# Performance work log

Measured on AMD Instinct MI355X. Metric: run time of the kernel, lower is better.

## Reference

```python
import jax, jax.numpy as jnp
import numpy as np

B, S, D, H = 2, 2048, 2048, 16
DH = D // H  # 128


def setup_inputs() -> dict:
    key = jax.random.key(0)
    ks = jax.random.split(key, 7)
    x = jax.random.normal(ks[0], (B, S, D), dtype=jnp.float32)
    # causal mask [b, s, s], True = attend
    mask = jnp.broadcast_to(jnp.tril(jnp.ones((S, S), dtype=bool)), (B, S, S))
    scale = 1.0 / np.sqrt(D)
    Wq = jax.random.normal(ks[1], (D, H, DH), dtype=jnp.float32) * scale
    Wk = jax.random.normal(ks[2], (D, 1, DH), dtype=jnp.float32) * scale
    Wv = jax.random.normal(ks[3], (D, 1, DH), dtype=jnp.float32) * scale
    Wo = jax.random.normal(ks[4], (H, DH, D), dtype=jnp.float32) * scale
    bo = jnp.zeros((D,), dtype=jnp.float32)
    return {"x": x, "mask": mask, "Wq": Wq, "Wk": Wk, "Wv": Wv, "Wo": Wo, "bo": bo}


def reference(x, mask, Wq, Wk, Wv, Wo, bo):
    # projections: q [b,s,h,dh]; k,v [b,s,1,dh] (single shared KV head)
    q = jnp.einsum("bsd,dhe->bshe", x, Wq)
    k = jnp.einsum("bsd,dhe->bshe", x, Wk)[:, :, 0, :]  # [b,s,dh]
    v = jnp.einsum("bsd,dhe->bshe", x, Wv)[:, :, 0, :]  # [b,s,dh]
    # scores [b,h,s,s] with 1/sqrt(d_head) scaling
    scores = jnp.einsum("bqhe,bke->bhqk", q, k) / jnp.sqrt(
        jnp.asarray(q.shape[-1], dtype=q.dtype)
    )
    big_neg = jnp.finfo(scores.dtype).min
    scores = jnp.where(mask[:, None, :, :], scores, big_neg)
    probs = jax.nn.softmax(scores, axis=-1)
    attn = jnp.einsum("bhqk,bke->bhqe", probs, v)  # [b,h,s,dh]
    # output projection contracting (head, d_head) -> d_state, with bias
    out = jnp.einsum("bhqe,hed->bqd", attn, Wo) + bo
    return out
```

## Files before the change

### kernel.cpp

```cpp
#include <hip/hip_runtime.h>
#include <cmath>
#include <cstdint>

typedef __bf16 bf16;
typedef __bf16 bf16x8 __attribute__((ext_vector_type(8)));
typedef __bf16 bf16x4 __attribute__((ext_vector_type(4)));
typedef float f32x4 __attribute__((ext_vector_type(4)));

#define SDIM 2048
#define DDIM 2048
#define NQKV 2304
#define DH   128

__device__ __forceinline__ void glds16(const bf16* g, bf16* l) {
    __builtin_amdgcn_global_load_lds(
        (const __attribute__((address_space(1))) void*)g,
        (__attribute__((address_space(3))) void*)l, 16, 0, 0);
}

__global__ __launch_bounds__(256) void prep_kernel(const float* __restrict__ x,
                                                   const float* __restrict__ Wq,
                                                   const float* __restrict__ Wk,
                                                   const float* __restrict__ Wv,
                                                   const float* __restrict__ Wo,
                                                   bf16* __restrict__ xb,
                                                   bf16* __restrict__ Wqkv_t,
                                                   bf16* __restrict__ Wo_t) {
    __shared__ float tile[32][33];
    int bx = blockIdx.x;
    if (bx < 8192) {
        int i = bx * 256 + threadIdx.x;
        float4 v = reinterpret_cast<const float4*>(x)[i];
        bf16x4 o;
        o[0] = (bf16)v.x; o[1] = (bf16)v.y; o[2] = (bf16)v.z; o[3] = (bf16)v.w;
        reinterpret_cast<bf16x4*>(xb)[i] = o;
        return;
    }
    bx -= 8192;
    const float* src; bf16* dst; int srcN; int t;
    if (bx < 4096)      { src = Wq; dst = Wqkv_t;                      srcN = 2048; t = bx; }
    else if (bx < 4352) { src = Wk; dst = Wqkv_t + (size_t)2048*2048;  srcN = 128;  t = bx - 4096; }
    else if (bx < 4608) { src = Wv; dst = Wqkv_t + (size_t)2176*2048;  srcN = 128;  t = bx - 4352; }
    else                { src = Wo; dst = Wo_t;                        srcN = 2048; t = bx - 4608; }
    const int srcK = 2048;
    int ntx = srcN >> 5;
    int n0 = (t % ntx) * 32, k0 = (t / ntx) * 32;
    int tx = threadIdx.x & 31;
    int ty = threadIdx.x >> 5;
    for (int i = 0; i < 4; i++)
        tile[ty + i*8][tx] = src[(size_t)(k0 + ty + i*8) * srcN + n0 + tx];
    __syncthreads();
    for (int i = 0; i < 4; i++)
        dst[(size_t)(n0 + ty + i*8) * srcK + k0 + tx] = (bf16)tile[tx][ty + i*8];
}

__global__ __launch_bounds__(256) void vtrans_kernel(const bf16* __restrict__ QKV,
                                                     bf16* __restrict__ Vt) {
    __shared__ bf16 tile[32][33];
    int tx = threadIdx.x & 31;
    int ty = threadIdx.x >> 5;
    int d0 = blockIdx.x * 32;
    int s0 = blockIdx.y * 32;
    int b  = blockIdx.z;
    for (int i = 0; i < 4; i++)
        tile[ty + i*8][tx] = QKV[((size_t)b * SDIM + s0 + ty + i*8) * NQKV + 2176 + d0 + tx];
    __syncthreads();
    for (int i = 0; i < 4; i++)
        Vt[((size_t)b * DH + d0 + ty + i*8) * SDIM + s0 + tx] = tile[tx][ty + i*8];
}

template<int WRITE_F32>
__global__ __launch_bounds__(256) void gemm_bt_kernel(const bf16* __restrict__ A,
                                                      const bf16* __restrict__ Bt,
                                                      void* __restrict__ Cout,
                                                      const float* __restrict__ bias,
                                                      int K, int N) {
    __shared__ bf16 As[128 * 32];
    __shared__ bf16 Bs[128 * 32];
    const int tid  = threadIdx.x;
    const int wave = tid >> 6, lane = tid & 63;
    const int quad = lane >> 4, l15 = lane & 15;
    const int tm = blockIdx.x * 128, tn = blockIdx.y * 128;
    const int wm = (wave >> 1) * 64, wn = (wave & 1) * 64;

    const int lrow = lane >> 2, lcol = (lane & 3) * 8;
    const int wrow = wave * 32;
    const bf16* Ag0 = A  + (size_t)(tm + wrow + lrow)      * K + lcol;
    const bf16* Ag1 = A  + (size_t)(tm + wrow + 16 + lrow) * K + lcol;
    const bf16* Bg0 = Bt + (size_t)(tn + wrow + lrow)      * K + lcol;
    const bf16* Bg1 = Bt + (size_t)(tn + wrow + 16 + lrow) * K + lcol;
    bf16* Al0 = As + (wrow)      * 32;
    bf16* Al1 = As + (wrow + 16) * 32;
    bf16* Bl0 = Bs + (wrow)      * 32;
    bf16* Bl1 = Bs + (wrow + 16) * 32;

    f32x4 acc[4][4];
    for (int i = 0; i < 4; i++)
        for (int j = 0; j < 4; j++) acc[i][j] = (f32x4)0.0f;

    for (int k0 = 0; k0 < K; k0 += 32) {
        __syncthreads();
        glds16(Ag0 + k0, Al0);
        glds16(Ag1 + k0, Al1);
        glds16(Bg0 + k0, Bl0);
        glds16(Bg1 + k0, Bl1);
        __syncthreads();
        bf16x8 af[4], bfr[4];
        for (int i = 0; i < 4; i++)
            af[i]  = *reinterpret_cast<const bf16x8*>(As + (wm + i*16 + l15) * 32 + quad*8);
        for (int j = 0; j < 4; j++)
            bfr[j] = *reinterpret_cast<const bf16x8*>(Bs + (wn + j*16 + l15) * 32 + quad*8);
        for (int i = 0; i < 4; i++)
            for (int j = 0; j < 4; j++)
                acc[i][j] = __builtin_amdgcn_mfma_f32_16x16x32_bf16(af[i], bfr[j], acc[i][j], 0, 0, 0);
    }

    for (int i = 0; i < 4; i++)
        for (int j = 0; j < 4; j++)
            for (int r = 0; r < 4; r++) {
                int row = tm + wm + i*16 + quad*4 + r;
                int col = tn + wn + j*16 + l15;
                float v = acc[i][j][r];
                if (WRITE_F32)
                    reinterpret_cast<float*>(Cout)[(size_t)row * N + col] = v + bias[col];
                else
                    reinterpret_cast<bf16*>(Cout)[(size_t)row * N + col] = (bf16)v;
            }
}

#define FPLD 72

__global__ __launch_bounds__(512) void flash_kernel(const bf16* __restrict__ QKV,
                                                    const bf16* __restrict__ Vt,
                                                    bf16* __restrict__ attn) {
    __shared__ bf16 KVS[16384];
    __shared__ bf16 Ps[8 * 16 * FPLD];
    bf16* Ks  = KVS;
    bf16* Vts = KVS + 8192;

    const int tid  = threadIdx.x;
    const int wave = tid >> 6, lane = tid & 63;
    const int quad = lane >> 4, l15 = lane & 15;
    const int bx = blockIdx.x;
    const int qs = 255 - (bx >> 1);
    const int b  = bx & 1;
    const int q  = qs * 8 + wave;
    const size_t rowbase = (size_t)b * SDIM;
    const bf16* Vtb = Vt + (size_t)b * DH * SDIM;
    const float scale = 0.088388347648318447f;

    const int s0 = wave, s1 = wave + 8;
    const int krow0 = s0*4 + (lane >> 4), krow1 = s1*4 + (lane >> 4);
    const int kchunk = lane & 15;
    const bf16* kg0 = QKV + (rowbase + krow0) * NQKV + 2048 + ((kchunk ^ (krow0 & 15)) * 8);
    const bf16* kg1 = QKV + (rowbase + krow1) * NQKV + 2048 + ((kchunk ^ (krow1 & 15)) * 8);
    bf16* kl0 = Ks + s0 * 512;
    bf16* kl1 = Ks + s1 * 512;
    const int vrow0 = s0*8 + (lane >> 3), vrow1 = s1*8 + (lane >> 3);
    const int vchunk = lane & 7;
    const bf16* vg0 = Vtb + (size_t)vrow0 * SDIM + ((vchunk ^ (vrow0 & 7)) * 8);
    const bf16* vg1 = Vtb + (size_t)vrow1 * SDIM + ((vchunk ^ (vrow1 & 7)) * 8);
    bf16* vl0 = Vts + s0 * 512;
    bf16* vl1 = Vts + s1 * 512;

    bf16x8 qf[4];
    {
        const bf16* qp = QKV + (rowbase + q) * NQKV + l15 * DH + quad * 8;
        for (int kk = 0; kk < 4; kk++)
            qf[kk] = *reinterpret_cast<const bf16x8*>(qp + kk * 32);
    }
    float l_s[4] = {0.0f, 0.0f, 0.0f, 0.0f};
    f32x4 acc[8];
    for (int d = 0; d < 8; d++) acc[d] = (f32x4)0.0f;

    const int ntiles = (qs >> 3) + 1;
    bf16* Pw = Ps + wave * (16 * FPLD);

    const bf16* kp0 = kg0; const bf16* kp1 = kg1;
    const bf16* vp0 = vg0; const bf16* vp1 = vg1;

    for (int t = 0; t < ntiles; t++) {
        const int key0 = t * 64;
        __syncthreads();
        glds16(kp0, kl0); glds16(kp1, kl1);
        glds16(vp0, vl0); glds16(vp1, vl1);
        kp0 += 64 * NQKV; kp1 += 64 * NQKV; vp0 += 64; vp1 += 64;
        __syncthreads();

        f32x4 sc[4];
        for (int c = 0; c < 4; c++) sc[c] = (f32x4)0.0f;
        for (int c = 0; c < 4; c++)
            for (int kk = 0; kk < 4; kk++) {
                int j = (kk*4 + quad) ^ l15;
                bf16x8 kf = *reinterpret_cast<const bf16x8*>(
                    Ks + (c*16 + l15) * 128 + j * 8);
                sc[c] = __builtin_amdgcn_mfma_f32_16x16x32_bf16(qf[kk], kf, sc[c], 0, 0, 0);
            }

        const bool tail = (key0 + 63 > q);
        for (int c = 0; c < 4; c++)
            for (int r = 0; r < 4; r++) {
                float p;
                if (tail && (key0 + c*16 + l15 > q)) p = 0.0f;
                else p = __expf(sc[c][r] * scale);
                l_s[r] += p;
                Pw[(quad*4 + r) * FPLD + c*16 + l15] = (bf16)p;
            }

        for (int kk2 = 0; kk2 < 2; kk2++) {
            bf16x8 pf = *reinterpret_cast<const bf16x8*>(Pw + l15 * FPLD + kk2*32 + quad*8);
            for (int dd = 0; dd < 8; dd++) {
                int d = dd*16 + l15;
                int j = (kk2*4 + quad) ^ (l15 & 7);
                bf16x8 vf = *reinterpret_cast<const bf16x8*>(Vts + d * 64 + j * 8);
                acc[dd] = __builtin_amdgcn_mfma_f32_16x16x32_bf16(pf, vf, acc[dd], 0, 0, 0);
            }
        }
    }

    __syncthreads();

    for (int d = 1; d < 16; d <<= 1)
        for (int r = 0; r < 4; r++) l_s[r] += __shfl_xor(l_s[r], d);

    bf16* Ow = KVS + wave * 2048;
    for (int r = 0; r < 4; r++) {
        float inv = 1.0f / l_s[r];
        for (int d = 0; d < 8; d++)
            Ow[(quad*4 + r) * 128 + d*16 + l15] = (bf16)(acc[d][r] * inv);
    }
    const int orow = lane >> 2;
    const int ocol = (lane & 3) * 8;
    bf16* ob = attn + (rowbase + q) * (size_t)DDIM;
    for (int it = 0; it < 4; it++)
        *reinterpret_cast<uint4*>(ob + orow * DH + ocol + it*32) =
            *reinterpret_cast<const uint4*>(Ow + orow * 128 + ocol + it*32);
}

extern "C" void kernel_launch(void* const* d_in, const int* in_sizes, int n_in,
                              void* d_out, int out_size, void* d_ws, size_t ws_size,
                              hipStream_t stream) {
    const float* x  = (const float*)d_in[0];
    const float* Wq = (const float*)d_in[2];
    const float* Wk = (const float*)d_in[3];
    const float* Wv = (const float*)d_in[4];
    const float* Wo = (const float*)d_in[5];
    const float* bo = (const float*)d_in[6];
    float* out = (float*)d_out;

    char* ws = (char*)d_ws;
    bf16* xb     = (bf16*)(ws);
    bf16* Wqkv_t = (bf16*)(ws + 16777216);
    bf16* Wo_t   = (bf16*)(ws + 26214400);
    bf16* QKV    = (bf16*)(ws + 34603008);
    bf16* attn   = (bf16*)(ws + 53477376);
    bf16* Vtb    = (bf16*)(ws + 70254592);
    (void)ws_size; (void)in_sizes; (void)n_in; (void)out_size;

    prep_kernel<<<16896, 256, 0, stream>>>(x, Wq, Wk, Wv, Wo, xb, Wqkv_t, Wo_t);
    gemm_bt_kernel<0><<<dim3(32, 18), 256, 0, stream>>>(xb, Wqkv_t, (void*)QKV, nullptr, 2048, 2304);
    vtrans_kernel<<<dim3(4, 64, 2), 256, 0, stream>>>(QKV, Vtb);
    flash_kernel<<<512, 512, 0, stream>>>(QKV, Vtb, attn);
    gemm_bt_kernel<1><<<dim3(32, 16), 256, 0, stream>>>(attn, Wo_t, (void*)out, bo, 2048, 2048);
}
```

Baseline: 313.6 us.

## Double-buffer LDS tiles in GEMM and flash kernels; retile flash to 4 waves

Both the GEMM and the flash-attention kernels now use two LDS buffers. The next K/V (or A/B) tile is prefetched with global_load_lds while MFMAs work on the current one, which removes one barrier per iteration. The flash kernel also shrinks to 256 threads with 32-key tiles and 4 query rows per block, giving twice as many blocks. The costs are more LDS per block in the GEMM, smaller per-tile work in the flash kernel, and reliance on the barrier waiting for the async LDS loads to finish.

```diff
diff --git a/kernel.cpp b/kernel.cpp
--- a/kernel.cpp
+++ b/kernel.cpp
@@ -75,8 +75,8 @@
                                                       void* __restrict__ Cout,
                                                       const float* __restrict__ bias,
                                                       int K, int N) {
-    __shared__ bf16 As[128 * 32];
-    __shared__ bf16 Bs[128 * 32];
+    __shared__ bf16 As[2][128 * 32];
+    __shared__ bf16 Bs[2][128 * 32];
     const int tid  = threadIdx.x;
     const int wave = tid >> 6, lane = tid & 63;
     const int quad = lane >> 4, l15 = lane & 15;
@@ -89,27 +89,30 @@
     const bf16* Ag1 = A  + (size_t)(tm + wrow + 16 + lrow) * K + lcol;
     const bf16* Bg0 = Bt + (size_t)(tn + wrow + lrow)      * K + lcol;
     const bf16* Bg1 = Bt + (size_t)(tn + wrow + 16 + lrow) * K + lcol;
-    bf16* Al0 = As + (wrow)      * 32;
-    bf16* Al1 = As + (wrow + 16) * 32;
-    bf16* Bl0 = Bs + (wrow)      * 32;
-    bf16* Bl1 = Bs + (wrow + 16) * 32;
 
     f32x4 acc[4][4];
     for (int i = 0; i < 4; i++)
         for (int j = 0; j < 4; j++) acc[i][j] = (f32x4)0.0f;
 
+    glds16(Ag0, As[0] + wrow * 32);
+    glds16(Ag1, As[0] + (wrow + 16) * 32);
+    glds16(Bg0, Bs[0] + wrow * 32);
+    glds16(Bg1, Bs[0] + (wrow + 16) * 32);
+
     for (int k0 = 0; k0 < K; k0 += 32) {
+        const int buf = (k0 >> 5) & 1;
         __syncthreads();
-        glds16(Ag0 + k0, Al0);
-        glds16(Ag1 + k0, Al1);
-        glds16(Bg0 + k0, Bl0);
-        glds16(Bg1 + k0, Bl1);
-        __syncthreads();
+        if (k0 + 32 < K) {
+            glds16(Ag0 + k0 + 32, As[buf ^ 1] + wrow * 32);
+            glds16(Ag1 + k0 + 32, As[buf ^ 1] + (wrow + 16) * 32);
+            glds16(Bg0 + k0 + 32, Bs[buf ^ 1] + wrow * 32);
+            glds16(Bg1 + k0 + 32, Bs[buf ^ 1] + (wrow + 16) * 32);
+        }
         bf16x8 af[4], bfr[4];
         for (int i = 0; i < 4; i++)
-            af[i]  = *reinterpret_cast<const bf16x8*>(As + (wm + i*16 + l15) * 32 + quad*8);
+            af[i]  = *reinterpret_cast<const bf16x8*>(As[buf] + (wm + i*16 + l15) * 32 + quad*8);
         for (int j = 0; j < 4; j++)
-            bfr[j] = *reinterpret_cast<const bf16x8*>(Bs + (wn + j*16 + l15) * 32 + quad*8);
+            bfr[j] = *reinterpret_cast<const bf16x8*>(Bs[buf] + (wn + j*16 + l15) * 32 + quad*8);
         for (int i = 0; i < 4; i++)
             for (int j = 0; j < 4; j++)
                 acc[i][j] = __builtin_amdgcn_mfma_f32_16x16x32_bf16(af[i], bfr[j], acc[i][j], 0, 0, 0);
@@ -128,40 +131,36 @@
             }
 }
 
-#define FPLD 72
-
-__global__ __launch_bounds__(512) void flash_kernel(const bf16* __restrict__ QKV,
+#define FPLD 40
+
+__global__ __launch_bounds__(256) void flash_kernel(const bf16* __restrict__ QKV,
                                                     const bf16* __restrict__ Vt,
                                                     bf16* __restrict__ attn) {
-    __shared__ bf16 KVS[16384];
-    __shared__ bf16 Ps[8 * 16 * FPLD];
-    bf16* Ks  = KVS;
-    bf16* Vts = KVS + 8192;
+    __shared__ bf16 Ks[2][32 * 128];
+    __shared__ bf16 Vts[2][128 * 32];
+    __shared__ bf16 Ps[4 * 16 * FPLD];
 
     const int tid  = threadIdx.x;
     const int wave = tid >> 6, lane = tid & 63;
     const int quad = lane >> 4, l15 = lane & 15;
     const int bx = blockIdx.x;
-    const int qs = 255 - (bx >> 1);
+    const int qs = 511 - (bx >> 1);
     const int b  = bx & 1;
-    const int q  = qs * 8 + wave;
+    const int q  = qs * 4 + wave;
     const size_t rowbase = (size_t)b * SDIM;
     const bf16* Vtb = Vt + (size_t)b * DH * SDIM;
     const float scale = 0.088388347648318447f;
 
-    const int s0 = wave, s1 = wave + 8;
-    const int krow0 = s0*4 + (lane >> 4), krow1 = s1*4 + (lane >> 4);
+    const int ks0 = wave, ks1 = wave + 4;
+    const int krow0 = ks0*4 + (lane >> 4), krow1 = ks1*4 + (lane >> 4);
     const int kchunk = lane & 15;
     const bf16* kg0 = QKV + (rowbase + krow0) * NQKV + 2048 + ((kchunk ^ (krow0 & 15)) * 8);
     const bf16* kg1 = QKV + (rowbase + krow1) * NQKV + 2048 + ((kchunk ^ (krow1 & 15)) * 8);
-    bf16* kl0 = Ks + s0 * 512;
-    bf16* kl1 = Ks + s1 * 512;
-    const int vrow0 = s0*8 + (lane >> 3), vrow1 = s1*8 + (lane >> 3);
-    const int vchunk = lane & 7;
-    const bf16* vg0 = Vtb + (size_t)vrow0 * SDIM + ((vchunk ^ (vrow0 & 7)) * 8);
-    const bf16* vg1 = Vtb + (size_t)vrow1 * SDIM + ((vchunk ^ (vrow1 & 7)) * 8);
-    bf16* vl0 = Vts + s0 * 512;
-    bf16* vl1 = Vts + s1 * 512;
+    const int vrow0 = ks0*16 + (lane >> 2), vrow1 = ks1*16 + (lane >> 2);
+    const int vchunk = lane & 3;
+    const int vsw0 = (vrow0 ^ (vrow0 >> 2)) & 3, vsw1 = (vrow1 ^ (vrow1 >> 2)) & 3;
+    const bf16* vg0 = Vtb + (size_t)vrow0 * SDIM + ((vchunk ^ vsw0) * 8);
+    const bf16* vg1 = Vtb + (size_t)vrow1 * SDIM + ((vchunk ^ vsw1) * 8);
 
     bf16x8 qf[4];
     {
@@ -173,32 +172,39 @@
     f32x4 acc[8];
     for (int d = 0; d < 8; d++) acc[d] = (f32x4)0.0f;
 
-    const int ntiles = (qs >> 3) + 1;
+    const int ntiles = ((qs * 4 + 3) >> 5) + 1;
     bf16* Pw = Ps + wave * (16 * FPLD);
-
-    const bf16* kp0 = kg0; const bf16* kp1 = kg1;
-    const bf16* vp0 = vg0; const bf16* vp1 = vg1;
+    const int vswr = (l15 ^ (l15 >> 2)) & 3;
+
+    glds16(kg0, Ks[0] + ks0 * 512);
+    glds16(kg1, Ks[0] + ks1 * 512);
+    glds16(vg0, Vts[0] + ks0 * 512);
+    glds16(vg1, Vts[0] + ks1 * 512);
 
     for (int t = 0; t < ntiles; t++) {
-        const int key0 = t * 64;
+        const int key0 = t * 32;
+        const int buf = t & 1;
         __syncthreads();
-        glds16(kp0, kl0); glds16(kp1, kl1);
-        glds16(vp0, vl0); glds16(vp1, vl1);
-        kp0 += 64 * NQKV; kp1 += 64 * NQKV; vp0 += 64; vp1 += 64;
-        __syncthreads();
-
-        f32x4 sc[4];
-        for (int c = 0; c < 4; c++) sc[c] = (f32x4)0.0f;
-        for (int c = 0; c < 4; c++)
+        if (t + 1 < ntiles) {
+            const int nk = key0 + 32;
+            glds16(kg0 + (size_t)nk * NQKV, Ks[buf ^ 1] + ks0 * 512);
+            glds16(kg1 + (size_t)nk * NQKV, Ks[buf ^ 1] + ks1 * 512);
+            glds16(vg0 + nk, Vts[buf ^ 1] + ks0 * 512);
+            glds16(vg1 + nk, Vts[buf ^ 1] + ks1 * 512);
+        }
+
+        f32x4 sc[2];
+        sc[0] = (f32x4)0.0f; sc[1] = (f32x4)0.0f;
+        for (int c = 0; c < 2; c++)
             for (int kk = 0; kk < 4; kk++) {
                 int j = (kk*4 + quad) ^ l15;
                 bf16x8 kf = *reinterpret_cast<const bf16x8*>(
-                    Ks + (c*16 + l15) * 128 + j * 8);
+                    Ks[buf] + (c*16 + l15) * 128 + j * 8);
                 sc[c] = __builtin_amdgcn_mfma_f32_16x16x32_bf16(qf[kk], kf, sc[c], 0, 0, 0);
             }
 
-        const bool tail = (key0 + 63 > q);
-        for (int c = 0; c < 4; c++)
+        const bool tail = (key0 + 31 > q);
+        for (int c = 0; c < 2; c++)
             for (int r = 0; r < 4; r++) {
                 float p;
                 if (tail && (key0 + c*16 + l15 > q)) p = 0.0f;
@@ -207,12 +213,12 @@
                 Pw[(quad*4 + r) * FPLD + c*16 + l15] = (bf16)p;
             }
 
-        for (int kk2 = 0; kk2 < 2; kk2++) {
-            bf16x8 pf = *reinterpret_cast<const bf16x8*>(Pw + l15 * FPLD + kk2*32 + quad*8);
+        {
+            bf16x8 pf = *reinterpret_cast<const bf16x8*>(Pw + l15 * FPLD + quad*8);
             for (int dd = 0; dd < 8; dd++) {
-                int d = dd*16 + l15;
-                int j = (kk2*4 + quad) ^ (l15 & 7);
-                bf16x8 vf = *reinterpret_cast<const bf16x8*>(Vts + d * 64 + j * 8);
+                int j = quad ^ vswr;
+                bf16x8 vf = *reinterpret_cast<const bf16x8*>(
+                    Vts[buf] + (dd*16 + l15) * 32 + j * 8);
                 acc[dd] = __builtin_amdgcn_mfma_f32_16x16x32_bf16(pf, vf, acc[dd], 0, 0, 0);
             }
         }
@@ -223,7 +229,7 @@
     for (int d = 1; d < 16; d <<= 1)
         for (int r = 0; r < 4; r++) l_s[r] += __shfl_xor(l_s[r], d);
 
-    bf16* Ow = KVS + wave * 2048;
+    bf16* Ow = &Ks[0][0] + wave * 2048;
     for (int r = 0; r < 4; r++) {
         float inv = 1.0f / l_s[r];
         for (int d = 0; d < 8; d++)
@@ -260,6 +266,6 @@
     prep_kernel<<<16896, 256, 0, stream>>>(x, Wq, Wk, Wv, Wo, xb, Wqkv_t, Wo_t);
     gemm_bt_kernel<0><<<dim3(32, 18), 256, 0, stream>>>(xb, Wqkv_t, (void*)QKV, nullptr, 2048, 2304);
     vtrans_kernel<<<dim3(4, 64, 2), 256, 0, stream>>>(QKV, Vtb);
-    flash_kernel<<<512, 512, 0, stream>>>(QKV, Vtb, attn);
+    flash_kernel<<<1024, 256, 0, stream>>>(QKV, Vtb, attn);
     gemm_bt_kernel<1><<<dim3(32, 16), 256, 0, stream>>>(attn, Wo_t, (void*)out, bo, 2048, 2048);
 }
```

Measured after the change: 316.3 us. No clear change (+0.9%).
